# Performance work log

Measured on AMD Instinct MI355X. Metric: run time of the kernel, lower is better.

The kernel has to match this reference:

```python
import jax, jax.numpy as jnp
import numpy as np

EPS = 1e-5


def _bn(x, g, b, m, v):
    # eval-mode BatchNorm over the last (channel) axis
    return g * (x - m) * jax.lax.rsqrt(v + EPS) + b


def setup_inputs() -> dict:
    key = jax.random.key(0)
    ks = jax.random.split(key, 16)
    B, N, K, C, Cout, G = 2, 16384, 32, 64, 64, 10
    inp = {
        "points": jax.random.normal(ks[0], (B, N, 3), jnp.float32),
        "features": jax.random.normal(ks[1], (B, N, C), jnp.float32),
        "grouped_idx": jax.random.randint(ks[2], (B, N, K), 0, N, jnp.int32),
        # pos_proj: Conv2d(geo_ch, in_ch, 1) + BN + ReLU
        "W_pos": jax.random.normal(ks[3], (C, G), jnp.float32) / np.sqrt(G),
        "b_pos": jnp.zeros((C,), jnp.float32),
        "bn1_g": jnp.ones((C,), jnp.float32),
        "bn1_b": jnp.zeros((C,), jnp.float32),
        "bn1_m": jax.random.normal(ks[4], (C,), jnp.float32) * 0.1,
        "bn1_v": jax.random.uniform(ks[5], (C,), jnp.float32, 0.5, 1.5),
        # gcm_layer: Conv2d(in_ch, in_ch, 1) + BN + ReLU
        "W_gcm": jax.random.normal(ks[6], (C, C), jnp.float32) / np.sqrt(C),
        "b_gcm": jnp.zeros((C,), jnp.float32),
        "bn2_g": jnp.ones((C,), jnp.float32),
        "bn2_b": jnp.zeros((C,), jnp.float32),
        "bn2_m": jax.random.normal(ks[7], (C,), jnp.float32) * 0.1,
        "bn2_v": jax.random.uniform(ks[8], (C,), jnp.float32, 0.5, 1.5),
        # att_conv_catfea: Linear(nsample, 1)
        "W_att": jax.random.normal(ks[9], (K,), jnp.float32) / np.sqrt(K),
        "b_att": jnp.zeros((), jnp.float32),
        # out_layer: Linear(in_ch, out_ch) + LayerNorm + ReLU
        "W_out": jax.random.normal(ks[10], (Cout, C), jnp.float32) / np.sqrt(C),
        "b_out": jnp.zeros((Cout,), jnp.float32),
        "ln_g": jnp.ones((Cout,), jnp.float32),
        "ln_b": jnp.zeros((Cout,), jnp.float32),
    }
    return inp


def reference(points, features, grouped_idx, W_pos, b_pos, bn1_g, bn1_b, bn1_m, bn1_v,
              W_gcm, b_gcm, bn2_g, bn2_b, bn2_m, bn2_v, W_att, b_att,
              W_out, b_out, ln_g, ln_b):
    gather = jax.vmap(lambda arr, idx: arr[idx])  # [N,C],[N,K] -> [N,K,C]
    grouped_points = gather(points, grouped_idx)          # [B,N,K,3]
    grouped_f = gather(features, grouped_idx)             # [B,N,K,C]

    # legacy geometric encoding: [xi, xj, xi - xj, ||xi - xj||] -> geo_ch = 10
    xi = points[:, :, None, :]
    diff = xi - grouped_points
    dist = jnp.linalg.norm(diff, axis=-1, keepdims=True)
    geo = jnp.concatenate(
        [jnp.broadcast_to(xi, grouped_points.shape), grouped_points, diff, dist], axis=-1)

    # pos_proj: 1x1 conv == channel linear, + BN + ReLU
    expanded = jax.nn.relu(_bn(jnp.einsum('bnkg,cg->bnkc', geo, W_pos) + b_pos,
                               bn1_g, bn1_b, bn1_m, bn1_v))

    h = grouped_f + expanded
    # gcm_layer
    h = jax.nn.relu(_bn(jnp.einsum('bnkc,dc->bnkd', h, W_gcm) + b_gcm,
                        bn2_g, bn2_b, bn2_m, bn2_v))

    # attention over neighbor dim K -> score per channel, softmax over channels (dim=2 of [B,N,C,1])
    score = jnp.einsum('bnkc,k->bnc', h, W_att) + b_att   # [B,N,C]
    score = jax.nn.softmax(score, axis=-1)
    h = h * score[:, :, None, :]                          # [B,N,K,C]

    pooled = jnp.max(h, axis=2)                           # maxpooling downsample -> [B,N,C]
    res = pooled + features

    # out_layer: Linear + LayerNorm + ReLU
    y = jnp.einsum('bnc,oc->bno', res, W_out) + b_out
    mu = jnp.mean(y, axis=-1, keepdims=True)
    var = jnp.var(y, axis=-1, keepdims=True)
    y = ln_g * (y - mu) * jax.lax.rsqrt(var + EPS) + ln_b
    return jax.nn.relu(y)
```

## Files before the change

kernel.cpp:

```cpp
#include <hip/hip_runtime.h>
#include <hip/hip_bf16.h>

#define EPSF 1e-5f

typedef __attribute__((ext_vector_type(8))) short bf16x8;
typedef __attribute__((ext_vector_type(4))) float f32x4;
typedef __attribute__((ext_vector_type(2))) unsigned int u32x2;
typedef __attribute__((ext_vector_type(4))) unsigned int u32x4;
typedef __attribute__((ext_vector_type(4))) int i32x4;

constexpr int B_ = 2, N_ = 16384;
constexpr int HSTR = 72;
constexpr int RSTR = 72;
constexpr int PPW  = 16;
constexpr int NW   = 4;
constexpr int PPB  = 64;
constexpr int NWG  = (B_ * N_) / PPB;
constexpr int HALF = NWG / 2;
constexpr size_t PP_BYTES = (size_t)B_ * N_ * 16;

__device__ __forceinline__ short f2bf(float f) {
    __hip_bfloat16 h = __float2bfloat16(f);
    short s; __builtin_memcpy(&s, &h, 2); return s;
}
__device__ __forceinline__ unsigned int pkbf(float a, float b) {
    float2 f2; f2.x = a; f2.y = b;
    __hip_bfloat162 h = __float22bfloat162_rn(f2);
    unsigned int u; __builtin_memcpy(&u, &h, 4); return u;
}

__global__ __launch_bounds__(256) void prep_points(
    const float* __restrict__ pts, float* __restrict__ pp)
{
    const int i = blockIdx.x * 256 + threadIdx.x;
    if (i < B_ * N_) {
        f32x4 o = { pts[3 * i], pts[3 * i + 1], pts[3 * i + 2], 0.f };
        ((f32x4*)pp)[i] = o;
    }
}

template<bool PAD>
__global__ __launch_bounds__(256, 2) void bridgenet14(
    const float* __restrict__ points,
    const float* __restrict__ pp,
    const float* __restrict__ features,
    const int*   __restrict__ gidx,
    const float* __restrict__ Wpos,
    const float* __restrict__ bposv,
    const float* __restrict__ bn1g, const float* __restrict__ bn1b,
    const float* __restrict__ bn1m, const float* __restrict__ bn1v,
    const float* __restrict__ Wgcm,
    const float* __restrict__ bgcm,
    const float* __restrict__ bn2g, const float* __restrict__ bn2b,
    const float* __restrict__ bn2m, const float* __restrict__ bn2v,
    const float* __restrict__ Watt,
    const float* __restrict__ batt,
    const float* __restrict__ Wout,
    const float* __restrict__ bout,
    const float* __restrict__ lng, const float* __restrict__ lnb,
    float* __restrict__ out)
{
    __shared__ __align__(16) short hbuf[NW][2][32 * HSTR];
    __shared__ __align__(16) short resstage[PPB * RSTR];
    __shared__ __align__(16) short wb2[8 * 64 * 8];
    __shared__ __align__(16) short wb3[8 * 64 * 8];

    const int t    = threadIdx.x;
    const int w    = t >> 6;
    const int l    = t & 63;
    const int l15  = l & 15;
    const int quad = l >> 4;
    const int c4   = l15 * 4;

    const int wg  = blockIdx.x;
    const int blk = ((wg & 7) >> 2) * HALF + ((wg >> 3) << 2) + (wg & 3);

    {
        #pragma unroll
        for (int u = 0; u < 4; ++u) {
            const int s  = w * 4 + u;
            const int nt = (s >> 1) & 3, ks = s & 1;
            const float* src = (s < 8 ? Wgcm : Wout) + (c4 + nt) * 64 + ks * 32 + quad * 8;
            const f32x4 w0 = *(const f32x4*)src;
            const f32x4 w1 = *(const f32x4*)(src + 4);
            bf16x8 f;
            #pragma unroll
            for (int j = 0; j < 4; ++j) {
                f[j]     = f2bf(w0[j]);
                f[j + 4] = f2bf(w1[j]);
            }
            short* dst = (s < 8 ? wb2 : wb3);
            *(bf16x8*)&dst[((s & 7) * 64 + l) * 8] = f;
        }
    }

    bf16x8 bposf[4];
    #pragma unroll
    for (int nt = 0; nt < 4; ++nt) {
        const int c = c4 + nt;
        #pragma unroll
        for (int j = 0; j < 8; ++j) {
            const int g = quad * 8 + j;
            bposf[nt][j] = f2bf(g < 10 ? Wpos[c * 10 + g] : 0.f);
        }
    }
    f32x4 ps1, pb1, ps2, pb2;
    {
        const f32x4 g1 = *(const f32x4*)(bn1g + c4);
        const f32x4 b1 = *(const f32x4*)(bn1b + c4);
        const f32x4 m1 = *(const f32x4*)(bn1m + c4);
        const f32x4 v1 = *(const f32x4*)(bn1v + c4);
        const f32x4 bp = *(const f32x4*)(bposv + c4);
        const f32x4 g2 = *(const f32x4*)(bn2g + c4);
        const f32x4 b2 = *(const f32x4*)(bn2b + c4);
        const f32x4 m2 = *(const f32x4*)(bn2m + c4);
        const f32x4 v2 = *(const f32x4*)(bn2v + c4);
        const f32x4 bg = *(const f32x4*)(bgcm + c4);
        #pragma unroll
        for (int j = 0; j < 4; ++j) {
            ps1[j] = g1[j] * rsqrtf(v1[j] + EPSF);
            pb1[j] = ps1[j] * (bp[j] - m1[j]) + b1[j];
            ps2[j] = g2[j] * rsqrtf(v2[j] + EPSF);
            pb2[j] = ps2[j] * (bg[j] - m2[j]) + b2[j];
        }
    }
    float wat[2][4];
    #pragma unroll
    for (int mt = 0; mt < 2; ++mt)
        #pragma unroll
        for (int r = 0; r < 4; ++r)
            wat[mt][r] = Watt[mt * 16 + quad * 4 + r];
    const float battv = batt[0];

    const f32x4 zero4 = {0.f, 0.f, 0.f, 0.f};
    const int base = blk * PPB + w * PPW;
    const int bb   = ((blk * PPB) >> 14) * N_;

    const float* __restrict__ fb  = features + (size_t)bb * 64;
    const float* __restrict__ ppb = pp + (size_t)bb * 4;
    const int*   __restrict__ gb  = gidx + (size_t)base * 32;

    auto LOADI = [&](int i, i32x4 (&gi)[2]) {
        gi[0] = *(const i32x4*)(gb + i * 32 + quad * 4);
        gi[1] = *(const i32x4*)(gb + i * 32 + 16 + quad * 4);
    };
    auto LOADD = [&](int i, const i32x4 (&gi)[2],
                     f32x4 (&f4)[2][4], bf16x8 (&ageo)[2], f32x4& resid) {
        #pragma unroll
        for (int mt = 0; mt < 2; ++mt)
            #pragma unroll
            for (int r = 0; r < 4; ++r)
                f4[mt][r] = *(const f32x4*)(fb + (((unsigned)gi[mt][r]) << 6) + c4);
        const int pt = base + i;
        resid = *(const f32x4*)(features + (size_t)pt * 64 + c4);
        int gv[2];
        gv[0] = gb[i * 32 + l15];
        gv[1] = gb[i * 32 + 16 + l15];
        float xi0, xi1, xi2, px[2], py[2], pz[2];
        if (PAD) {
            const f32x4 x4 = *(const f32x4*)(pp + (size_t)pt * 4);
            xi0 = x4[0]; xi1 = x4[1]; xi2 = x4[2];
            #pragma unroll
            for (int mt = 0; mt < 2; ++mt) {
                const f32x4 p4 = *(const f32x4*)(ppb + (((unsigned)gv[mt]) << 2));
                px[mt] = p4[0]; py[mt] = p4[1]; pz[mt] = p4[2];
            }
        } else {
            xi0 = points[(size_t)pt * 3];
            xi1 = points[(size_t)pt * 3 + 1];
            xi2 = points[(size_t)pt * 3 + 2];
            #pragma unroll
            for (int mt = 0; mt < 2; ++mt) {
                const float* ppt = points + (size_t)(bb + gv[mt]) * 3;
                px[mt] = ppt[0]; py[mt] = ppt[1]; pz[mt] = ppt[2];
            }
        }
        #pragma unroll
        for (int mt = 0; mt < 2; ++mt) {
            const float dx = xi0 - px[mt], dy = xi1 - py[mt], dz = xi2 - pz[mt];
            const float dist = __builtin_amdgcn_sqrtf(dx * dx + dy * dy + dz * dz);
            u32x4 u = {0u, 0u, 0u, 0u};
            if (quad == 0) {
                u[0] = pkbf(xi0, xi1); u[1] = pkbf(xi2, px[mt]);
                u[2] = pkbf(py[mt], pz[mt]); u[3] = pkbf(dx, dy);
            } else if (quad == 1) {
                u[0] = pkbf(dz, dist);
            }
            __builtin_memcpy(&ageo[mt], &u, 16);
        }
    };

    auto FRONT = [&](short* hb, const f32x4 (&f4)[2][4], const bf16x8 (&ageo)[2],
                     f32x4 (&acc2)[2][4]) {
        __builtin_amdgcn_s_setprio(1);
        f32x4 acc1[2][4];
        #pragma unroll
        for (int mt = 0; mt < 2; ++mt)
            #pragma unroll
            for (int nt = 0; nt < 4; ++nt)
                acc1[mt][nt] = __builtin_amdgcn_mfma_f32_16x16x32_bf16(
                    ageo[mt], bposf[nt], zero4, 0, 0, 0);
        __builtin_amdgcn_s_setprio(0);

        #pragma unroll
        for (int mt = 0; mt < 2; ++mt)
            #pragma unroll
            for (int r = 0; r < 4; ++r) {
                const int k = mt * 16 + quad * 4 + r;
                float v[4];
                #pragma unroll
                for (int j = 0; j < 4; ++j)
                    v[j] = f4[mt][r][j] + fmaxf(ps1[j] * acc1[mt][j][r] + pb1[j], 0.f);
                u32x2 hv = { pkbf(v[0], v[1]), pkbf(v[2], v[3]) };
                *(u32x2*)&hb[k * HSTR + c4] = hv;
            }

        bf16x8 a2[2][2];
        #pragma unroll
        for (int mt = 0; mt < 2; ++mt)
            #pragma unroll
            for (int ks = 0; ks < 2; ++ks)
                a2[mt][ks] = *(const bf16x8*)&hb[(mt * 16 + l15) * HSTR + ks * 32 + quad * 8];
        __builtin_amdgcn_s_setprio(1);
        #pragma unroll
        for (int nt = 0; nt < 4; ++nt) {
            const bf16x8 b0 = *(const bf16x8*)&wb2[((nt * 2 + 0) * 64 + l) * 8];
            const bf16x8 b1 = *(const bf16x8*)&wb2[((nt * 2 + 1) * 64 + l) * 8];
            #pragma unroll
            for (int mt = 0; mt < 2; ++mt) {
                f32x4 a = __builtin_amdgcn_mfma_f32_16x16x32_bf16(a2[mt][0], b0, zero4, 0, 0, 0);
                acc2[mt][nt] = __builtin_amdgcn_mfma_f32_16x16x32_bf16(a2[mt][1], b1, a, 0, 0, 0);
            }
        }
        __builtin_amdgcn_s_setprio(0);
    };

    auto BACK = [&](int i, const f32x4 (&acc2)[2][4], const f32x4& resid) {
        float res[4];
        {
            float sp[4], mk[4];
            #pragma unroll
            for (int nt = 0; nt < 4; ++nt) {
                sp[nt] = 0.f; mk[nt] = 0.f;
                #pragma unroll
                for (int mt = 0; mt < 2; ++mt)
                    #pragma unroll
                    for (int r = 0; r < 4; ++r) {
                        const float h2 = fmaxf(ps2[nt] * acc2[mt][nt][r] + pb2[nt], 0.f);
                        sp[nt] += h2 * wat[mt][r];
                        mk[nt] = fmaxf(mk[nt], h2);
                    }
                sp[nt] += __shfl_xor(sp[nt], 16);
                sp[nt] += __shfl_xor(sp[nt], 32);
                mk[nt] = fmaxf(mk[nt], __shfl_xor(mk[nt], 16));
                mk[nt] = fmaxf(mk[nt], __shfl_xor(mk[nt], 32));
            }
            float e[4], s = 0.f;
            #pragma unroll
            for (int nt = 0; nt < 4; ++nt) { e[nt] = __expf(sp[nt] + battv); s += e[nt]; }
            #pragma unroll
            for (int o = 1; o < 16; o <<= 1) s += __shfl_xor(s, o);
            const float inv = __builtin_amdgcn_rcpf(s);
            #pragma unroll
            for (int nt = 0; nt < 4; ++nt)
                res[nt] = e[nt] * inv * mk[nt] + resid[nt];
        }
        if (quad == 0) {
            u32x2 rv = { pkbf(res[0], res[1]), pkbf(res[2], res[3]) };
            *(u32x2*)&resstage[(w * PPW + i) * RSTR + c4] = rv;
        }
    };

    short* hb0 = &hbuf[w][0][0];
    short* hb1 = &hbuf[w][1][0];

    i32x4 giA0[2], giA1[2], giB0[2], giB1[2];
    LOADI(0, giA0); LOADI(1, giA1);
    LOADI(2, giB0); LOADI(3, giB1);
    f32x4  f4A0[2][4], f4A1[2][4], f4B0[2][4], f4B1[2][4];
    bf16x8 agA0[2], agA1[2], agB0[2], agB1[2];
    f32x4  rsA0, rsA1, rsB0, rsB1;
    LOADD(0, giA0, f4A0, agA0, rsA0);
    LOADD(1, giA1, f4A1, agA1, rsA1);

    __syncthreads();

    #pragma unroll
    for (int ip = 0; ip < PPW; ip += 4) {
        f32x4 accA0[2][4], accA1[2][4];
        FRONT(hb0, f4A0, agA0, accA0);
        FRONT(hb1, f4A1, agA1, accA1);
        if (ip + 2 < PPW) {
            LOADD(ip + 2, giB0, f4B0, agB0, rsB0);
            LOADD(ip + 3, giB1, f4B1, agB1, rsB1);
            if (ip + 4 < PPW) { LOADI(ip + 4, giA0); LOADI(ip + 5, giA1); }
        }
        BACK(ip, accA0, rsA0);
        BACK(ip + 1, accA1, rsA1);

        if (ip + 2 < PPW) {
            f32x4 accB0[2][4], accB1[2][4];
            FRONT(hb0, f4B0, agB0, accB0);
            FRONT(hb1, f4B1, agB1, accB1);
            if (ip + 4 < PPW) {
                LOADD(ip + 4, giA0, f4A0, agA0, rsA0);
                LOADD(ip + 5, giA1, f4A1, agA1, rsA1);
                if (ip + 6 < PPW) { LOADI(ip + 6, giB0); LOADI(ip + 7, giB1); }
            }
            BACK(ip + 2, accB0, rsB0);
            BACK(ip + 3, accB1, rsB1);
        }
    }

    __syncthreads();

    {
        const f32x4 lngv  = *(const f32x4*)(lng + c4);
        const f32x4 lnbv  = *(const f32x4*)(lnb + c4);
        const f32x4 boutv = *(const f32x4*)(bout + c4);
        bf16x8 a3[2];
        #pragma unroll
        for (int ks = 0; ks < 2; ++ks)
            a3[ks] = *(const bf16x8*)&resstage[(w * 16 + l15) * RSTR + ks * 32 + quad * 8];
        f32x4 acc3[4];
        #pragma unroll
        for (int nt = 0; nt < 4; ++nt) {
            const bf16x8 b0 = *(const bf16x8*)&wb3[((nt * 2 + 0) * 64 + l) * 8];
            const bf16x8 b1 = *(const bf16x8*)&wb3[((nt * 2 + 1) * 64 + l) * 8];
            f32x4 a = __builtin_amdgcn_mfma_f32_16x16x32_bf16(a3[0], b0, zero4, 0, 0, 0);
            acc3[nt] = __builtin_amdgcn_mfma_f32_16x16x32_bf16(a3[1], b1, a, 0, 0, 0);
        }
        #pragma unroll
        for (int u = 0; u < 4; ++u) {
            float y[4], s = 0.f;
            #pragma unroll
            for (int nt = 0; nt < 4; ++nt) { y[nt] = acc3[nt][u] + boutv[nt]; s += y[nt]; }
            #pragma unroll
            for (int o = 1; o < 16; o <<= 1) s += __shfl_xor(s, o);
            const float mu = s * (1.f / 64.f);
            float dv[4], v2 = 0.f;
            #pragma unroll
            for (int nt = 0; nt < 4; ++nt) { dv[nt] = y[nt] - mu; v2 += dv[nt] * dv[nt]; }
            #pragma unroll
            for (int o = 1; o < 16; o <<= 1) v2 += __shfl_xor(v2, o);
            const float rs = rsqrtf(v2 * (1.f / 64.f) + EPSF);
            const int pto = blk * PPB + w * 16 + quad * 4 + u;
            f32x4 ov;
            #pragma unroll
            for (int nt = 0; nt < 4; ++nt)
                ov[nt] = fmaxf(lngv[nt] * dv[nt] * rs + lnbv[nt], 0.f);
            *(f32x4*)(out + (size_t)pto * 64 + c4) = ov;
        }
    }
}

extern "C" void kernel_launch(void* const* d_in, const int* in_sizes, int n_in,
                              void* d_out, int out_size, void* d_ws, size_t ws_size,
                              hipStream_t stream) {
    const float* points   = (const float*)d_in[0];
    const float* features = (const float*)d_in[1];
    const int*   gidxp    = (const int*)d_in[2];
    const bool   pad      = (ws_size >= PP_BYTES);
    float* pp = (float*)d_ws;
    if (pad) {
        hipLaunchKernelGGL(prep_points, dim3((B_ * N_ + 255) / 256), dim3(256), 0, stream,
                           points, pp);
        hipLaunchKernelGGL((bridgenet14<true>), dim3(NWG), dim3(256), 0, stream,
            points, pp, features, gidxp,
            (const float*)d_in[3],  (const float*)d_in[4],
            (const float*)d_in[5],  (const float*)d_in[6],  (const float*)d_in[7],  (const float*)d_in[8],
            (const float*)d_in[9],  (const float*)d_in[10],
            (const float*)d_in[11], (const float*)d_in[12], (const float*)d_in[13], (const float*)d_in[14],
            (const float*)d_in[15], (const float*)d_in[16],
            (const float*)d_in[17], (const float*)d_in[18],
            (const float*)d_in[19], (const float*)d_in[20],
            (float*)d_out);
    } else {
        hipLaunchKernelGGL((bridgenet14<false>), dim3(NWG), dim3(256), 0, stream,
            points, pp, features, gidxp,
            (const float*)d_in[3],  (const float*)d_in[4],
            (const float*)d_in[5],  (const float*)d_in[6],  (const float*)d_in[7],  (const float*)d_in[8],
            (const float*)d_in[9],  (const float*)d_in[10],
            (const float*)d_in[11], (const float*)d_in[12], (const float*)d_in[13], (const float*)d_in[14],
            (const float*)d_in[15], (const float*)d_in[16],
            (const float*)d_in[17], (const float*)d_in[18],
            (const float*)d_in[19], (const float*)d_in[20],
            (float*)d_out);
    }
}
```

Baseline: 152.5 us.

## Batch softmax reductions across four points and restructure load pipeline

```diff
diff --git a/kernel.cpp b/kernel.cpp
--- a/kernel.cpp
+++ b/kernel.cpp
@@ -40,7 +40,7 @@
 }
 
 template<bool PAD>
-__global__ __launch_bounds__(256, 2) void bridgenet14(
+__global__ __launch_bounds__(256, 2) void bridgenet15(
     const float* __restrict__ points,
     const float* __restrict__ pp,
     const float* __restrict__ features,
@@ -190,8 +190,8 @@
         }
     };
 
-    auto FRONT = [&](short* hb, const f32x4 (&f4)[2][4], const bf16x8 (&ageo)[2],
-                     f32x4 (&acc2)[2][4]) {
+    auto FRONTR = [&](short* hb, const f32x4 (&f4)[2][4], const bf16x8 (&ageo)[2],
+                      float (&sp)[4], float (&mk)[4]) {
         __builtin_amdgcn_s_setprio(1);
         f32x4 acc1[2][4];
         #pragma unroll
@@ -222,6 +222,7 @@
             for (int ks = 0; ks < 2; ++ks)
                 a2[mt][ks] = *(const bf16x8*)&hb[(mt * 16 + l15) * HSTR + ks * 32 + quad * 8];
         __builtin_amdgcn_s_setprio(1);
+        f32x4 acc2[2][4];
         #pragma unroll
         for (int nt = 0; nt < 4; ++nt) {
             const bf16x8 b0 = *(const bf16x8*)&wb2[((nt * 2 + 0) * 64 + l) * 8];
@@ -233,41 +234,60 @@
             }
         }
         __builtin_amdgcn_s_setprio(0);
+
+        #pragma unroll
+        for (int nt = 0; nt < 4; ++nt) {
+            sp[nt] = 0.f; mk[nt] = 0.f;
+            #pragma unroll
+            for (int mt = 0; mt < 2; ++mt)
+                #pragma unroll
+                for (int r = 0; r < 4; ++r) {
+                    const float h2 = fmaxf(ps2[nt] * acc2[mt][nt][r] + pb2[nt], 0.f);
+                    sp[nt] += h2 * wat[mt][r];
+                    mk[nt] = fmaxf(mk[nt], h2);
+                }
+        }
     };
 
-    auto BACK = [&](int i, const f32x4 (&acc2)[2][4], const f32x4& resid) {
-        float res[4];
-        {
-            float sp[4], mk[4];
+    auto BACKQ = [&](int i0, float (&sp)[4][4], float (&mk)[4][4],
+                     const f32x4& r0, const f32x4& r1,
+                     const f32x4& r2, const f32x4& r3) {
+        #pragma unroll
+        for (int j = 0; j < 4; ++j)
             #pragma unroll
             for (int nt = 0; nt < 4; ++nt) {
-                sp[nt] = 0.f; mk[nt] = 0.f;
-                #pragma unroll
-                for (int mt = 0; mt < 2; ++mt)
-                    #pragma unroll
-                    for (int r = 0; r < 4; ++r) {
-                        const float h2 = fmaxf(ps2[nt] * acc2[mt][nt][r] + pb2[nt], 0.f);
-                        sp[nt] += h2 * wat[mt][r];
-                        mk[nt] = fmaxf(mk[nt], h2);
-                    }
-                sp[nt] += __shfl_xor(sp[nt], 16);
-                sp[nt] += __shfl_xor(sp[nt], 32);
-                mk[nt] = fmaxf(mk[nt], __shfl_xor(mk[nt], 16));
-                mk[nt] = fmaxf(mk[nt], __shfl_xor(mk[nt], 32));
-            }
-            float e[4], s = 0.f;
-            #pragma unroll
-            for (int nt = 0; nt < 4; ++nt) { e[nt] = __expf(sp[nt] + battv); s += e[nt]; }
-            #pragma unroll
-            for (int o = 1; o < 16; o <<= 1) s += __shfl_xor(s, o);
-            const float inv = __builtin_amdgcn_rcpf(s);
+                sp[j][nt] += __shfl_xor(sp[j][nt], 16);
+                sp[j][nt] += __shfl_xor(sp[j][nt], 32);
+                mk[j][nt] = fmaxf(mk[j][nt], __shfl_xor(mk[j][nt], 16));
+                mk[j][nt] = fmaxf(mk[j][nt], __shfl_xor(mk[j][nt], 32));
+            }
+        float e[4][4], s[4];
+        #pragma unroll
+        for (int j = 0; j < 4; ++j) {
+            s[j] = 0.f;
+            #pragma unroll
+            for (int nt = 0; nt < 4; ++nt) {
+                e[j][nt] = __expf(sp[j][nt] + battv);
+                s[j] += e[j][nt];
+            }
+        }
+        #pragma unroll
+        for (int o = 1; o < 16; o <<= 1)
+            #pragma unroll
+            for (int j = 0; j < 4; ++j)
+                s[j] += __shfl_xor(s[j], o);
+        const f32x4* rs[4] = { &r0, &r1, &r2, &r3 };
+        #pragma unroll
+        for (int j = 0; j < 4; ++j) {
+            const float inv = __builtin_amdgcn_rcpf(s[j]);
+            float res[4];
             #pragma unroll
             for (int nt = 0; nt < 4; ++nt)
-                res[nt] = e[nt] * inv * mk[nt] + resid[nt];
-        }
-        if (quad == 0) {
-            u32x2 rv = { pkbf(res[0], res[1]), pkbf(res[2], res[3]) };
-            *(u32x2*)&resstage[(w * PPW + i) * RSTR + c4] = rv;
+                res[nt] = e[j][nt] * inv * mk[j][nt] + (*rs[j])[nt];
+            if (quad == 0) {
+                u32x2 rv = { pkbf(res[0], res[1]), pkbf(res[2], res[3]) };
+                *(u32x2*)&resstage[(w * PPW + i0 + j) * RSTR + c4] = rv;
+            }
         }
     };
 
@@ -275,41 +295,37 @@
     short* hb1 = &hbuf[w][1][0];
 
     i32x4 giA0[2], giA1[2], giB0[2], giB1[2];
-    LOADI(0, giA0); LOADI(1, giA1);
-    LOADI(2, giB0); LOADI(3, giB1);
+    LOADI(0, giA0); LOADI(1, giA1); LOADI(2, giB0); LOADI(3, giB1);
     f32x4  f4A0[2][4], f4A1[2][4], f4B0[2][4], f4B1[2][4];
     bf16x8 agA0[2], agA1[2], agB0[2], agB1[2];
-    f32x4  rsA0, rsA1, rsB0, rsB1;
-    LOADD(0, giA0, f4A0, agA0, rsA0);
-    LOADD(1, giA1, f4A1, agA1, rsA1);
+    f32x4  rA0, rA1, rB0, rB1, rN0, rN1;
+    LOADD(0, giA0, f4A0, agA0, rA0);
+    LOADD(1, giA1, f4A1, agA1, rA1);
 
     __syncthreads();
 
-    #pragma unroll
     for (int ip = 0; ip < PPW; ip += 4) {
-        f32x4 accA0[2][4], accA1[2][4];
-        FRONT(hb0, f4A0, agA0, accA0);
-        FRONT(hb1, f4A1, agA1, accA1);
-        if (ip + 2 < PPW) {
-            LOADD(ip + 2, giB0, f4B0, agB0, rsB0);
-            LOADD(ip + 3, giB1, f4B1, agB1, rsB1);
-            if (ip + 4 < PPW) { LOADI(ip + 4, giA0); LOADI(ip + 5, giA1); }
-        }
-        BACK(ip, accA0, rsA0);
-        BACK(ip + 1, accA1, rsA1);
-
-        if (ip + 2 < PPW) {
-            f32x4 accB0[2][4], accB1[2][4];
-            FRONT(hb0, f4B0, agB0, accB0);
-            FRONT(hb1, f4B1, agB1, accB1);
-            if (ip + 4 < PPW) {
-                LOADD(ip + 4, giA0, f4A0, agA0, rsA0);
-                LOADD(ip + 5, giA1, f4A1, agA1, rsA1);
-                if (ip + 6 < PPW) { LOADI(ip + 6, giB0); LOADI(ip + 7, giB1); }
-            }
-            BACK(ip + 2, accB0, rsB0);
-            BACK(ip + 3, accB1, rsB1);
-        }
+        float sp[4][4], mk[4][4];
+
+        LOADD(ip + 2, giB0, f4B0, agB0, rB0);
+        LOADD(ip + 3, giB1, f4B1, agB1, rB1);
+        if (ip + 4 < PPW) { LOADI(ip + 4, giA0); LOADI(ip + 5, giA1); }
+
+        FRONTR(hb0, f4A0, agA0, sp[0], mk[0]);
+        FRONTR(hb1, f4A1, agA1, sp[1], mk[1]);
+
+        if (ip + 4 < PPW) {
+            LOADD(ip + 4, giA0, f4A0, agA0, rN0);
+            LOADD(ip + 5, giA1, f4A1, agA1, rN1);
+            LOADI(ip + 6, giB0); LOADI(ip + 7, giB1);
+        }
+
+        FRONTR(hb0, f4B0, agB0, sp[2], mk[2]);
+        FRONTR(hb1, f4B1, agB1, sp[3], mk[3]);
+
+        BACKQ(ip, sp, mk, rA0, rA1, rB0, rB1);
+
+        rA0 = rN0; rA1 = rN1;
     }
 
     __syncthreads();
@@ -365,7 +381,7 @@
     if (pad) {
         hipLaunchKernelGGL(prep_points, dim3((B_ * N_ + 255) / 256), dim3(256), 0, stream,
                            points, pp);
-        hipLaunchKernelGGL((bridgenet14<true>), dim3(NWG), dim3(256), 0, stream,
+        hipLaunchKernelGGL((bridgenet15<true>), dim3(NWG), dim3(256), 0, stream,
             points, pp, features, gidxp,
             (const float*)d_in[3],  (const float*)d_in[4],
             (const float*)d_in[5],  (const float*)d_in[6],  (const float*)d_in[7],  (const float*)d_in[8],
@@ -376,7 +392,7 @@
             (const float*)d_in[19], (const float*)d_in[20],
             (float*)d_out);
     } else {
-        hipLaunchKernelGGL((bridgenet14<false>), dim3(NWG), dim3(256), 0, stream,
+        hipLaunchKernelGGL((bridgenet15<false>), dim3(NWG), dim3(256), 0, stream,
             points, pp, features, gidxp,
             (const float*)d_in[3],  (const float*)d_in[4],
             (const float*)d_in[5],  (const float*)d_in[6],  (const float*)d_in[7],  (const float*)d_in[8],
```

New measurement: 248.3 us. +62.9%, slower.
